# Optimization experiments

Hardware: AMD Instinct MI355X
Metric: run time of the kernel (lower is better)

Reference implementation:

```python
import jax, jax.numpy as jnp
import numpy as np

N = 100000
E = 1600000
G = 64  # number of graphs
EPS = 1e-5
NEG_SLOPE = 0.2


def _gat_conv(x, W, a_src, a_dst, b, src, dst, n, H, C):
    # x: [n, in]; W: [in, H*C]; a_src/a_dst: [H, C]; b: [H*C]
    h = (x @ W).reshape(n, H, C)                      # [n,H,C]
    al_s = jnp.sum(h * a_src, axis=-1)                # [n,H]
    al_d = jnp.sum(h * a_dst, axis=-1)                # [n,H]
    score = jax.nn.leaky_relu(al_s[src] + al_d[dst], NEG_SLOPE)  # [E,H]
    # segment softmax over incoming edges of each dst node
    m = jax.ops.segment_max(score, dst, num_segments=n)
    ex = jnp.exp(score - jax.lax.stop_gradient(m)[dst])
    den = jax.ops.segment_sum(ex, dst, num_segments=n)
    alpha = ex / den[dst]                             # [E,H]
    out = jax.ops.segment_sum(alpha[:, :, None] * h[src], dst, num_segments=n)
    return out.reshape(n, H * C) + b


def _bn_relu(x, gamma, beta):
    mu = jnp.mean(x, axis=0)
    var = jnp.var(x, axis=0)  # biased, matches torch BN normalization
    return jax.nn.relu((x - mu) * jax.lax.rsqrt(var + EPS) * gamma + beta)


def setup_inputs() -> dict:
    key = jax.random.key(0)
    ks = jax.random.split(key, 32)
    d = {}
    d['x'] = jax.random.normal(ks[0], (N, 3), dtype=jnp.float32)
    d['edge_index'] = jax.random.randint(ks[1], (2, E), 0, N, dtype=jnp.int64)
    d['batch'] = jnp.sort(jax.random.randint(ks[2], (N,), 0, G, dtype=jnp.int64))
    def p(k, shape):
        return jax.random.normal(k, shape, dtype=jnp.float32) * 0.1
    # conv1: 3 -> 16, heads=2
    d['W1'] = p(ks[3], (3, 32)); d['as1'] = p(ks[4], (2, 16)); d['ad1'] = p(ks[5], (2, 16)); d['b1'] = p(ks[6], (32,))
    d['g1'] = jnp.ones((32,), jnp.float32); d['be1'] = jnp.zeros((32,), jnp.float32)
    # conv2: 32 -> 32, heads=2
    d['W2'] = p(ks[7], (32, 64)); d['as2'] = p(ks[8], (2, 32)); d['ad2'] = p(ks[9], (2, 32)); d['b2'] = p(ks[10], (64,))
    d['g2'] = jnp.ones((64,), jnp.float32); d['be2'] = jnp.zeros((64,), jnp.float32)
    # conv3: 64 -> 64, heads=2
    d['W3'] = p(ks[11], (64, 128)); d['as3'] = p(ks[12], (2, 64)); d['ad3'] = p(ks[13], (2, 64)); d['b3'] = p(ks[14], (128,))
    d['g3'] = jnp.ones((128,), jnp.float32); d['be3'] = jnp.zeros((128,), jnp.float32)
    d['fcw'] = p(ks[15], (128, 10)); d['fcb'] = p(ks[16], (10,))
    return d


def reference(x, edge_index, batch, W1, as1, ad1, b1, g1, be1, W2, as2, ad2, b2, g2, be2, W3, as3, ad3, b3, g3, be3, fcw, fcb):
    n = x.shape[0]
    loops = jnp.arange(n, dtype=edge_index.dtype)  # PyG GATConv add_self_loops=True
    src = jnp.concatenate([edge_index[0], loops])
    dst = jnp.concatenate([edge_index[1], loops])
    h = _bn_relu(_gat_conv(x, W1, as1, ad1, b1, src, dst, n, 2, 16), g1, be1)
    h = _bn_relu(_gat_conv(h, W2, as2, ad2, b2, src, dst, n, 2, 32), g2, be2)
    h = _bn_relu(_gat_conv(h, W3, as3, ad3, b3, src, dst, n, 2, 64), g3, be3)
    pooled = jax.ops.segment_max(h, batch, num_segments=G)  # [G,128]
    return pooled @ fcw + fcb
```

## Files before the change

### kernel.cpp

```cpp
#include <hip/hip_runtime.h>
#include <cstddef>

constexpr int NN = 100000;
constexpr int NE = 1600000;
constexpr int TE = NE + NN;
constexpr int NG = 64;
constexpr float EPS = 1e-5f;
constexpr float NEG_SLOPE = 0.2f;
constexpr int NREP = 16;

constexpr int NBUCK = 256;
constexpr int DPB = 391;
constexpr int PHB = 256;
constexpr int CH = (TE + PHB - 1) / PHB;

typedef __attribute__((ext_vector_type(8))) short bf16x8;
typedef __attribute__((ext_vector_type(4))) float f32x4;

__device__ __forceinline__ unsigned short f2bf(float f) {
    unsigned u = __float_as_uint(f);
    u += 0x7fffu + ((u >> 16) & 1u);
    return (unsigned short)(u >> 16);
}
__device__ __forceinline__ float bf2f(unsigned short s) {
    return __uint_as_float((unsigned)s << 16);
}
__device__ __forceinline__ float bflo(unsigned u) { return __uint_as_float(u << 16); }
__device__ __forceinline__ float bfhi(unsigned u) { return __uint_as_float(u & 0xffff0000u); }
__device__ __forceinline__ void unpack8(uint4 v, float* f) {
    f[0] = bflo(v.x); f[1] = bfhi(v.x); f[2] = bflo(v.y); f[3] = bfhi(v.y);
    f[4] = bflo(v.z); f[5] = bfhi(v.z); f[6] = bflo(v.w); f[7] = bfhi(v.w);
}
__device__ __forceinline__ uint4 pack8(const float* o) {
    uint4 pk;
    pk.x = (unsigned)f2bf(o[0]) | ((unsigned)f2bf(o[1]) << 16);
    pk.y = (unsigned)f2bf(o[2]) | ((unsigned)f2bf(o[3]) << 16);
    pk.z = (unsigned)f2bf(o[4]) | ((unsigned)f2bf(o[5]) << 16);
    pk.w = (unsigned)f2bf(o[6]) | ((unsigned)f2bf(o[7]) << 16);
    return pk;
}
__device__ __forceinline__ bf16x8 ld_bf8(const unsigned short* p) {
    union { uint4 u; bf16x8 b; } cv;
    cv.u = *(const uint4*)p;
    return cv.b;
}
__device__ __forceinline__ float lrelu(float v) { return v > 0.f ? v : NEG_SLOPE * v; }


__global__ void k_hist(const int* __restrict__ ei, int* __restrict__ hist) {
    __shared__ int hcnt[NBUCK];
    for (int i = threadIdx.x; i < NBUCK; i += 256) hcnt[i] = 0;
    __syncthreads();
    int k = blockIdx.x;
    int e0 = k * CH, e1 = min(e0 + CH, TE);
    for (int e = e0 + threadIdx.x; e < e1; e += 256) {
        int d = (e < NE) ? ei[NE + e] : (e - NE);
        atomicAdd(&hcnt[d / DPB], 1);
    }
    __syncthreads();
    for (int b = threadIdx.x; b < NBUCK; b += 256) hist[b * PHB + k] = hcnt[b];
}

__global__ void k_scanA(int* __restrict__ hist, int* __restrict__ bsum) {
    __shared__ int ls[PHB];
    int b = blockIdx.x, t = threadIdx.x;
    int v = hist[b * PHB + t];
    ls[t] = v;
    __syncthreads();
    for (int off = 1; off < PHB; off <<= 1) {
        int add = (t >= off) ? ls[t - off] : 0;
        __syncthreads();
        ls[t] += add;
        __syncthreads();
    }
    hist[b * PHB + t] = ls[t] - v;
    if (t == PHB - 1) bsum[b] = ls[t];
}

__global__ void k_scanB(const int* __restrict__ bsum, int* __restrict__ bbase,
                        int* __restrict__ rowptr) {
    __shared__ int ls[NBUCK];
    int t = threadIdx.x;
    int v = bsum[t];
    ls[t] = v;
    __syncthreads();
    for (int off = 1; off < NBUCK; off <<= 1) {
        int add = (t >= off) ? ls[t - off] : 0;
        __syncthreads();
        ls[t] += add;
        __syncthreads();
    }
    bbase[t] = ls[t] - v;
    if (t == NBUCK - 1) { bbase[NBUCK] = ls[t]; rowptr[NN] = ls[t]; }
}

__global__ void k_scatter(const int* __restrict__ ei, const int* __restrict__ hist,
                          const int* __restrict__ bbase, int* __restrict__ pairs) {
    __shared__ int cur[NBUCK];
    int k = blockIdx.x;
    for (int b = threadIdx.x; b < NBUCK; b += 256) cur[b] = bbase[b] + hist[b * PHB + k];
    __syncthreads();
    int e0 = k * CH, e1 = min(e0 + CH, TE);
    for (int e = e0 + threadIdx.x; e < e1; e += 256) {
        int s, d;
        if (e < NE) { s = ei[e]; d = ei[NE + e]; } else { s = e - NE; d = s; }
        int b = d / DPB, ld = d - b * DPB;
        int pos = atomicAdd(&cur[b], 1);
        pairs[pos] = (s << 9) | ld;
    }
}

__global__ void k_csr(const int* __restrict__ pairs, const int* __restrict__ bbase,
                      int* __restrict__ rowptr, int* __restrict__ colsrc) {
    __shared__ int deg[DPB];
    __shared__ int exc[DPB];
    __shared__ int sc[512];
    int b = blockIdx.x, t = threadIdx.x;
    int base = bbase[b], cnt = bbase[b + 1] - base;
    int d0 = b * DPB;
    int ndst = min(DPB, NN - d0);
    for (int i = t; i < DPB; i += 256) deg[i] = 0;
    __syncthreads();
    for (int i = t; i < cnt; i += 256) atomicAdd(&deg[pairs[base + i] & 511], 1);
    __syncthreads();
    sc[t] = (t < DPB) ? deg[t] : 0;
    sc[t + 256] = (t + 256 < DPB) ? deg[t + 256] : 0;
    __syncthreads();
    for (int off = 1; off < 512; off <<= 1) {
        int a0 = (t >= off) ? sc[t - off] : 0;
        int a1 = (t + 256 >= off) ? sc[t + 256 - off] : 0;
        __syncthreads();
        sc[t] += a0; sc[t + 256] += a1;
        __syncthreads();
    }
    if (t < DPB) exc[t] = sc[t] - deg[t];
    if (t + 256 < DPB) exc[t + 256] = sc[t + 256] - deg[t + 256];
    __syncthreads();
    for (int i = t; i < ndst; i += 256) rowptr[d0 + i] = base + exc[i];
    for (int i = t; i < DPB; i += 256) deg[i] = 0;
    __syncthreads();
    for (int i = t; i < cnt; i += 256) {
        int p = pairs[base + i];
        int ld = p & 511;
        int s = (unsigned)p >> 9;
        int pos = base + exc[ld] + atomicAdd(&deg[ld], 1);
        colsrc[pos] = s;
    }
}


__global__ void k_wa(const float* __restrict__ W1, const float* __restrict__ as1,
                     const float* __restrict__ ad1,
                     const float* __restrict__ W2, const float* __restrict__ as2,
                     const float* __restrict__ ad2,
                     const float* __restrict__ W3, const float* __restrict__ as3,
                     const float* __restrict__ ad3,
                     float* __restrict__ was1, float* __restrict__ wad1,
                     float* __restrict__ was2, float* __restrict__ wad2,
                     float* __restrict__ was3, float* __restrict__ wad3) {
    int t = threadIdx.x;
    if (t < 6) {
        int h = t / 3, i = t % 3;
        float s = 0.f, d = 0.f;
        for (int c = 0; c < 16; ++c) {
            float w = W1[i * 32 + h * 16 + c];
            s += w * as1[h * 16 + c];
            d += w * ad1[h * 16 + c];
        }
        was1[t] = s; wad1[t] = d;
    }
    if (t < 64) {
        int h = t / 32, i = t % 32;
        float s = 0.f, d = 0.f;
        for (int c = 0; c < 32; ++c) {
            float w = W2[i * 64 + h * 32 + c];
            s += w * as2[h * 32 + c];
            d += w * ad2[h * 32 + c];
        }
        was2[t] = s; wad2[t] = d;
    }
    if (t < 128) {
        int h = t / 64, i = t % 64;
        float s = 0.f, d = 0.f;
        for (int c = 0; c < 64; ++c) {
            float w = W3[i * 128 + h * 64 + c];
            s += w * as3[h * 64 + c];
            d += w * ad3[h * 64 + c];
        }
        was3[t] = s; wad3[t] = d;
    }
}


__global__ void k_wsplit(const float* __restrict__ W2, const float* __restrict__ W3,
                         unsigned short* __restrict__ w2hi, unsigned short* __restrict__ w2lo,
                         unsigned short* __restrict__ w3hi, unsigned short* __restrict__ w3lo) {
    int t = blockIdx.x * 256 + threadIdx.x;
    if (t < 2048) {
        int c = t / 32, i = t % 32;
        float w = W2[i * 64 + c];
        unsigned short hi = f2bf(w);
        float lo = w - bf2f(hi);
        w2hi[c * 32 + i] = hi;
        w2lo[c * 32 + i] = f2bf(lo);
    }
    if (t < 8192) {
        int c = t / 64, i = t % 64;
        float w = W3[i * 128 + c];
        unsigned short hi = f2bf(w);
        float lo = w - bf2f(hi);
        w3hi[c * 64 + i] = hi;
        w3lo[c * 64 + i] = f2bf(lo);
    }
}


__global__ void k_logits1(const float* __restrict__ x, const float* __restrict__ was,
                          const float* __restrict__ wad, float* __restrict__ als,
                          float* __restrict__ ald) {
    int n = blockIdx.x * 256 + threadIdx.x;
    if (n >= NN) return;
    float x0 = x[n * 3], x1 = x[n * 3 + 1], x2 = x[n * 3 + 2];
    als[n * 2 + 0] = x0 * was[0] + x1 * was[1] + x2 * was[2];
    als[n * 2 + 1] = x0 * was[3] + x1 * was[4] + x2 * was[5];
    ald[n * 2 + 0] = x0 * wad[0] + x1 * wad[1] + x2 * wad[2];
    ald[n * 2 + 1] = x0 * wad[3] + x1 * wad[4] + x2 * wad[5];
}


template <int IN>
__global__ void k_prep(const unsigned short* __restrict__ x,
                       const float* __restrict__ bnrep,
                       const float* __restrict__ gamma, const float* __restrict__ beta,
                       const float* __restrict__ was, const float* __restrict__ wad,
                       unsigned short* __restrict__ xbn,
                       float* __restrict__ als, float* __restrict__ ald) {
    constexpr int P = IN / 8;
    __shared__ float sbn[2 * IN];
    __shared__ float swa[4 * IN];
    if (threadIdx.x < IN) {
        int c = threadIdx.x;
        float s = 0.f, ss = 0.f;
#pragma unroll
        for (int r = 0; r < NREP; ++r) {
            s  += bnrep[r * 2 * IN + c];
            ss += bnrep[r * 2 * IN + IN + c];
        }
        float mu = s / NN;
        float var = ss / NN - mu * mu;
        float sca = gamma[c] * rsqrtf(var + EPS);
        sbn[c] = sca;
        sbn[IN + c] = beta[c] - mu * sca;
    }
    for (int i = threadIdx.x; i < 2 * IN; i += 256) {
        swa[i] = was[i];
        swa[2 * IN + i] = wad[i];
    }
    __syncthreads();
    int idx = blockIdx.x * 256 + threadIdx.x;
    int node = idx / P, pl = idx % P;
    if (node >= NN) return;
    uint4 v = *(const uint4*)&x[(size_t)node * IN + pl * 8];
    float f[8];
    unpack8(v, f);
    float s0 = 0.f, s1 = 0.f, d0 = 0.f, d1 = 0.f;
#pragma unroll
    for (int k = 0; k < 8; ++k) {
        int c = pl * 8 + k;
        float t = f[k] * sbn[c] + sbn[IN + c];
        t = t > 0.f ? t : 0.f;
        f[k] = t;
        s0 += t * swa[c];           s1 += t * swa[IN + c];
        d0 += t * swa[2 * IN + c];  d1 += t * swa[3 * IN + c];
    }
    *(uint4*)&xbn[(size_t)node * IN + pl * 8] = pack8(f);
#pragma unroll
    for (int m = 1; m < P; m <<= 1) {
        s0 += __shfl_xor(s0, m, 64); s1 += __shfl_xor(s1, m, 64);
        d0 += __shfl_xor(d0, m, 64); d1 += __shfl_xor(d1, m, 64);
    }
    if (pl == 0) {
        als[node * 2 + 0] = s0; als[node * 2 + 1] = s1;
        ald[node * 2 + 0] = d0; ald[node * 2 + 1] = d1;
    }
}


template <int IN>
__global__ void k_agg(const int* __restrict__ rowptr, const int* __restrict__ colsrc,
                      const unsigned short* __restrict__ x,
                      const float* __restrict__ als, const float* __restrict__ ald,
                      unsigned short* __restrict__ agg) {
    constexpr int LPE = IN / 8;
    constexpr int EPI2 = 32 / LPE;
    constexpr int UNR = 2;
    __shared__ float4 etab[4][64];
    int wv = threadIdx.x >> 6, lane = threadIdx.x & 63;
    int hw = lane >> 5, hl = lane & 31;
    int base = ((int)blockIdx.x * 4 + wv) * 2;
    int wid = base + hw;
    bool valid = wid < NN;
    int start = 0, cnt = 0;
    float2 dv = make_float2(0.f, 0.f);
    if (valid) {
        start = rowptr[wid];
        cnt = rowptr[wid + 1] - start;
        dv = ((const float2*)ald)[wid];
    }
    int mc = max(cnt, __shfl_xor(cnt, 32, 64));

    if (mc <= 32) {
        int e = start + hl;
        bool act = valid && (hl < cnt);
        int s = act ? colsrc[e] : 0;
        float2 av = act ? ((const float2*)als)[s] : make_float2(0.f, 0.f);
        float t0 = act ? lrelu(av.x + dv.x) : -1e30f;
        float t1 = act ? lrelu(av.y + dv.y) : -1e30f;
        float m0 = t0, m1 = t1;
#pragma unroll
        for (int off = 16; off; off >>= 1) {
            m0 = fmaxf(m0, __shfl_xor(m0, off, 32));
            m1 = fmaxf(m1, __shfl_xor(m1, off, 32));
        }
        float w0 = act ? __expf(t0 - m0) : 0.f;
        float w1 = act ? __expf(t1 - m1) : 0.f;
        float den0 = w0, den1 = w1;
#pragma unroll
        for (int off = 16; off; off >>= 1) {
            den0 += __shfl_xor(den0, off, 32);
            den1 += __shfl_xor(den1, off, 32);
        }
        float i0 = valid ? 1.f / den0 : 0.f;
        float i1 = valid ? 1.f / den1 : 0.f;
        etab[wv][lane] = make_float4(__int_as_float(s), w0 * i0, w1 * i1, 0.f);
        int sub = hl / LPE, cl = hl % LPE;
        float a0[8], a1[8];
#pragma unroll
        for (int k = 0; k < 8; ++k) { a0[k] = 0.f; a1[k] = 0.f; }
        if (valid) {
            int cm1 = cnt - 1;
            for (int j0 = 0; j0 < cnt; j0 += EPI2 * UNR) {
                float l0[UNR], l1[UNR];
                uint4 hv[UNR];
#pragma unroll
                for (int u = 0; u < UNR; ++u) {
                    int jj = j0 + u * EPI2 + sub;
                    int jc = min(jj, cm1);
                    float4 ed = etab[wv][hw * 32 + jc];
                    bool on = jj <= cm1;
                    l0[u] = on ? ed.y : 0.f;
                    l1[u] = on ? ed.z : 0.f;
                    hv[u] = *(const uint4*)&x[(size_t)__float_as_int(ed.x) * IN + cl * 8];
                }
#pragma unroll
                for (int u = 0; u < UNR; ++u) {
                    float f[8];
                    unpack8(hv[u], f);
#pragma unroll
                    for (int k = 0; k < 8; ++k) {
                        a0[k] += l0[u] * f[k];
                        a1[k] += l1[u] * f[k];
                    }
                }
            }
        }
#pragma unroll
        for (int m = LPE; m < 32; m <<= 1) {
#pragma unroll
            for (int k = 0; k < 8; ++k) {
                a0[k] += __shfl_xor(a0[k], m, 64);
                a1[k] += __shfl_xor(a1[k], m, 64);
            }
        }
        if (valid && sub == 0) {
            *(uint4*)&agg[(size_t)wid * 2 * IN + cl * 8] = pack8(a0);
            *(uint4*)&agg[(size_t)wid * 2 * IN + IN + cl * 8] = pack8(a1);
        }
    } else {
        for (int i2 = 0; i2 < 2; ++i2) {
            int w2 = base + i2;
            if (w2 >= NN) continue;
            int st = rowptr[w2], en = rowptr[w2 + 1];
            float2 dv2 = ((const float2*)ald)[w2];
            float m0 = -1e30f, m1 = -1e30f;
            for (int e = st + lane; e < en; e += 64) {
                int s = colsrc[e];
                m0 = fmaxf(m0, lrelu(als[s * 2 + 0] + dv2.x));
                m1 = fmaxf(m1, lrelu(als[s * 2 + 1] + dv2.y));
            }
#pragma unroll
            for (int off = 32; off; off >>= 1) {
                m0 = fmaxf(m0, __shfl_xor(m0, off, 64));
                m1 = fmaxf(m1, __shfl_xor(m1, off, 64));
            }
            float den0 = 0.f, den1 = 0.f;
            for (int e = st + lane; e < en; e += 64) {
                int s = colsrc[e];
                den0 += __expf(lrelu(als[s * 2 + 0] + dv2.x) - m0);
                den1 += __expf(lrelu(als[s * 2 + 1] + dv2.y) - m1);
            }
#pragma unroll
            for (int off = 32; off; off >>= 1) {
                den0 += __shfl_xor(den0, off, 64);
                den1 += __shfl_xor(den1, off, 64);
            }
            float inv0 = 1.f / den0, inv1 = 1.f / den1;
            int c = lane;
            float a0 = 0.f, a1 = 0.f;
            for (int e = st; e < en; ++e) {
                int s = colsrc[e];
                float aa0 = __expf(lrelu(als[s * 2 + 0] + dv2.x) - m0) * inv0;
                float aa1 = __expf(lrelu(als[s * 2 + 1] + dv2.y) - m1) * inv1;
                if (c < IN) {
                    float vv = bf2f(x[(size_t)s * IN + c]);
                    a0 += aa0 * vv;
                    a1 += aa1 * vv;
                }
            }
            if (c < IN) {
                agg[(size_t)w2 * 2 * IN + c] = f2bf(a0);
                agg[(size_t)w2 * 2 * IN + IN + c] = f2bf(a1);
            }
        }
    }
}

__global__ void k_agg1(const int* __restrict__ rowptr, const int* __restrict__ colsrc,
                       const float* __restrict__ x, const float* __restrict__ als,
                       const float* __restrict__ ald, float* __restrict__ agg) {
    int wv = threadIdx.x >> 6, lane = threadIdx.x & 63;
    int hw = lane >> 5, hl = lane & 31;
    int base = ((int)blockIdx.x * 4 + wv) * 2;
    int wid = base + hw;
    bool valid = wid < NN;
    int start = 0, cnt = 0;
    float2 dv = make_float2(0.f, 0.f);
    if (valid) {
        start = rowptr[wid];
        cnt = rowptr[wid + 1] - start;
        dv = ((const float2*)ald)[wid];
    }
    int mc = max(cnt, __shfl_xor(cnt, 32, 64));
    if (mc <= 32) {
        int e = start + hl;
        bool act = valid && (hl < cnt);
        int s = act ? colsrc[e] : 0;
        float2 av = act ? ((const float2*)als)[s] : make_float2(0.f, 0.f);
        float t0 = act ? lrelu(av.x + dv.x) : -1e30f;
        float t1 = act ? lrelu(av.y + dv.y) : -1e30f;
        float m0 = t0, m1 = t1;
#pragma unroll
        for (int off = 16; off; off >>= 1) {
            m0 = fmaxf(m0, __shfl_xor(m0, off, 32));
            m1 = fmaxf(m1, __shfl_xor(m1, off, 32));
        }
        float w0 = act ? __expf(t0 - m0) : 0.f;
        float w1 = act ? __expf(t1 - m1) : 0.f;
        float den0 = w0, den1 = w1;
#pragma unroll
        for (int off = 16; off; off >>= 1) {
            den0 += __shfl_xor(den0, off, 32);
            den1 += __shfl_xor(den1, off, 32);
        }
        float a[6];
#pragma unroll
        for (int k = 0; k < 6; ++k) a[k] = 0.f;
        if (act) {
            float al0 = w0 / den0, al1 = w1 / den1;
            float x0 = x[s * 3], x1 = x[s * 3 + 1], x2 = x[s * 3 + 2];
            a[0] = al0 * x0; a[1] = al0 * x1; a[2] = al0 * x2;
            a[3] = al1 * x0; a[4] = al1 * x1; a[5] = al1 * x2;
        }
#pragma unroll
        for (int m = 1; m < 32; m <<= 1) {
#pragma unroll
            for (int k = 0; k < 6; ++k) a[k] += __shfl_xor(a[k], m, 64);
        }
        if (valid && hl == 0) {
#pragma unroll
            for (int k = 0; k < 6; ++k) agg[(size_t)wid * 6 + k] = a[k];
        }
    } else {
        for (int i2 = 0; i2 < 2; ++i2) {
            int w2 = base + i2;
            if (w2 >= NN) continue;
            int st = rowptr[w2], en = rowptr[w2 + 1];
            float2 dv2 = ((const float2*)ald)[w2];
            float m0 = -1e30f, m1 = -1e30f;
            for (int e = st + lane; e < en; e += 64) {
                int s = colsrc[e];
                m0 = fmaxf(m0, lrelu(als[s * 2 + 0] + dv2.x));
                m1 = fmaxf(m1, lrelu(als[s * 2 + 1] + dv2.y));
            }
#pragma unroll
            for (int off = 32; off; off >>= 1) {
                m0 = fmaxf(m0, __shfl_xor(m0, off, 64));
                m1 = fmaxf(m1, __shfl_xor(m1, off, 64));
            }
            float den0 = 0.f, den1 = 0.f;
            for (int e = st + lane; e < en; e += 64) {
                int s = colsrc[e];
                den0 += __expf(lrelu(als[s * 2 + 0] + dv2.x) - m0);
                den1 += __expf(lrelu(als[s * 2 + 1] + dv2.y) - m1);
            }
#pragma unroll
            for (int off = 32; off; off >>= 1) {
                den0 += __shfl_xor(den0, off, 64);
                den1 += __shfl_xor(den1, off, 64);
            }
            float inv0 = 1.f / den0, inv1 = 1.f / den1;
            float a[6];
#pragma unroll
            for (int k = 0; k < 6; ++k) a[k] = 0.f;
            for (int e = st + lane; e < en; e += 64) {
                int s = colsrc[e];
                float aa0 = __expf(lrelu(als[s * 2 + 0] + dv2.x) - m0) * inv0;
                float aa1 = __expf(lrelu(als[s * 2 + 1] + dv2.y) - m1) * inv1;
                float x0 = x[s * 3], x1 = x[s * 3 + 1], x2 = x[s * 3 + 2];
                a[0] += aa0 * x0; a[1] += aa0 * x1; a[2] += aa0 * x2;
                a[3] += aa1 * x0; a[4] += aa1 * x1; a[5] += aa1 * x2;
            }
#pragma unroll
            for (int m = 1; m < 64; m <<= 1) {
#pragma unroll
                for (int k = 0; k < 6; ++k) a[k] += __shfl_xor(a[k], m, 64);
            }
            if (lane == 0) {
#pragma unroll
                for (int k = 0; k < 6; ++k) agg[(size_t)w2 * 6 + k] = a[k];
            }
        }
    }
}


template <int IN, int OUT>
__global__ void k_tmfma(const unsigned short* __restrict__ agg,
                        const unsigned short* __restrict__ whi,
                        const unsigned short* __restrict__ wlo,
                        unsigned short* __restrict__ xout,
                        float* __restrict__ bnrep) {
    constexpr int C = OUT / 2;
    constexpr int NT = C / 16;
    constexpr int KS = IN / 32;
    __shared__ float red[2 * OUT];
    for (int i = threadIdx.x; i < 2 * OUT; i += 256) red[i] = 0.f;
    __syncthreads();
    int wv = threadIdx.x >> 6, l = threadIdx.x & 63;
    int head = wv & 1;
    int node0 = blockIdx.x * 32 + (wv >> 1) * 16;
    int lr = l & 15, kg = l >> 4;
    bf16x8 a[KS];
#pragma unroll
    for (int ks = 0; ks < KS; ++ks)
        a[ks] = ld_bf8(&agg[(size_t)(node0 + lr) * 2 * IN + head * IN + ks * 32 + kg * 8]);
    f32x4 acc[NT];
#pragma unroll
    for (int nt = 0; nt < NT; ++nt) acc[nt] = (f32x4){0.f, 0.f, 0.f, 0.f};
#pragma unroll
    for (int nt = 0; nt < NT; ++nt) {
        int ch = head * C + nt * 16 + lr;
#pragma unroll
        for (int ks = 0; ks < KS; ++ks) {
            bf16x8 bh = ld_bf8(&whi[(size_t)ch * IN + ks * 32 + kg * 8]);
            bf16x8 bl = ld_bf8(&wlo[(size_t)ch * IN + ks * 32 + kg * 8]);
            acc[nt] = __builtin_amdgcn_mfma_f32_16x16x32_bf16(a[ks], bh, acc[nt], 0, 0, 0);
            acc[nt] = __builtin_amdgcn_mfma_f32_16x16x32_bf16(a[ks], bl, acc[nt], 0, 0, 0);
        }
    }
#pragma unroll
    for (int nt = 0; nt < NT; ++nt) {
        int chO = head * C + nt * 16 + lr;
        float s = 0.f, ss = 0.f;
#pragma unroll
        for (int r = 0; r < 4; ++r) {
            float v = acc[nt][r];
            int node = node0 + kg * 4 + r;
            xout[(size_t)node * OUT + chO] = f2bf(v);
            s += v; ss += v * v;
        }
        atomicAdd(&red[chO], s);
        atomicAdd(&red[OUT + chO], ss);
    }
    __syncthreads();
    float* dst = &bnrep[(blockIdx.x & (NREP - 1)) * 2 * OUT];
    for (int i = threadIdx.x; i < 2 * OUT; i += 256) atomicAdd(&dst[i], red[i]);
}

__global__ void k_transform1(const float* __restrict__ agg, const float* __restrict__ W,
                             unsigned short* __restrict__ xout, float* __restrict__ bnrep,
                             int n) {
    __shared__ float xs[32 * 7];
    __shared__ float red[64];
    for (int i = threadIdx.x; i < 64; i += 256) red[i] = 0.f;
    int node0 = blockIdx.x * 32;
    for (int i = threadIdx.x; i < 192; i += 256) {
        int nn = node0 + i / 6;
        float v = (nn < n) ? agg[(size_t)node0 * 6 + i] : 0.f;
        xs[(i / 6) * 7 + (i % 6)] = v;
    }
    __syncthreads();
    int nl = threadIdx.x / 8, q = threadIdx.x % 8;
    int hd = (q >= 4);
    int node = node0 + nl;
    float4 acc = {0.f, 0.f, 0.f, 0.f};
#pragma unroll
    for (int i = 0; i < 3; ++i) {
        float xv = xs[nl * 7 + hd * 3 + i];
        float4 w = *(const float4*)&W[i * 32 + q * 4];
        acc.x += xv * w.x; acc.y += xv * w.y; acc.z += xv * w.z; acc.w += xv * w.w;
    }
    if (node < n) {
        uint2 pk;
        pk.x = (unsigned)f2bf(acc.x) | ((unsigned)f2bf(acc.y) << 16);
        pk.y = (unsigned)f2bf(acc.z) | ((unsigned)f2bf(acc.w) << 16);
        *(uint2*)&xout[(size_t)node * 32 + q * 4] = pk;
        atomicAdd(&red[q * 4 + 0], acc.x); atomicAdd(&red[32 + q * 4 + 0], acc.x * acc.x);
        atomicAdd(&red[q * 4 + 1], acc.y); atomicAdd(&red[32 + q * 4 + 1], acc.y * acc.y);
        atomicAdd(&red[q * 4 + 2], acc.z); atomicAdd(&red[32 + q * 4 + 2], acc.z * acc.z);
        atomicAdd(&red[q * 4 + 3], acc.w); atomicAdd(&red[32 + q * 4 + 3], acc.w * acc.w);
    }
    __syncthreads();
    float* dst = &bnrep[(blockIdx.x & (NREP - 1)) * 64];
    for (int i = threadIdx.x; i < 64; i += 256) atomicAdd(&dst[i], red[i]);
}


__global__ void k_pool(const unsigned short* __restrict__ h, const int* __restrict__ batch,
                       const float* __restrict__ bnrep, const float* __restrict__ gamma,
                       const float* __restrict__ beta, float* __restrict__ pooled, int n) {
    const int K = 32;
    int c = threadIdx.x;
    float s = 0.f, ss = 0.f;
#pragma unroll
    for (int r = 0; r < NREP; ++r) {
        s  += bnrep[r * 256 + c];
        ss += bnrep[r * 256 + 128 + c];
    }
    float mu = s / n;
    float var = ss / n - mu * mu;
    float scale = gamma[c] * rsqrtf(var + EPS);
    float shift = beta[c] - mu * scale;
    int n0 = blockIdx.x * K;
    if (n0 >= n) return;
    int nend = min(n, n0 + K);
    int curg = batch[n0];
    float m = 0.f;
    for (int nn = n0; nn < nend; ++nn) {
        int g = batch[nn];
        if (g != curg) {
            atomicMax((int*)&pooled[curg * 128 + c], __float_as_int(m));
            m = 0.f; curg = g;
        }
        float v = bf2f(h[(size_t)nn * 128 + c]) * scale + shift;
        m = fmaxf(m, v > 0.f ? v : 0.f);
    }
    atomicMax((int*)&pooled[curg * 128 + c], __float_as_int(m));
}

__global__ void k_fc(const float* __restrict__ pooled, const float* __restrict__ fcw,
                     const float* __restrict__ fcb, float* __restrict__ out) {
    int t = threadIdx.x;
    if (t >= NG * 10) return;
    int g = t / 10, j = t % 10;
    float acc = fcb[j];
#pragma unroll
    for (int c = 0; c < 128; ++c) acc += pooled[g * 128 + c] * fcw[c * 10 + j];
    out[g * 10 + j] = acc;
}


extern "C" void kernel_launch(void* const* d_in, const int* in_sizes, int n_in,
                              void* d_out, int out_size, void* d_ws, size_t ws_size,
                              hipStream_t stream) {
    const float* x   = (const float*)d_in[0];
    const int*   ei  = (const int*)d_in[1];
    const int*   bat = (const int*)d_in[2];
    const float* W1  = (const float*)d_in[3];
    const float* as1 = (const float*)d_in[4];
    const float* ad1 = (const float*)d_in[5];
    const float* g1  = (const float*)d_in[7];
    const float* be1 = (const float*)d_in[8];
    const float* W2  = (const float*)d_in[9];
    const float* as2 = (const float*)d_in[10];
    const float* ad2 = (const float*)d_in[11];
    const float* g2  = (const float*)d_in[13];
    const float* be2 = (const float*)d_in[14];
    const float* W3  = (const float*)d_in[15];
    const float* as3 = (const float*)d_in[16];
    const float* ad3 = (const float*)d_in[17];
    const float* g3  = (const float*)d_in[19];
    const float* be3 = (const float*)d_in[20];
    const float* fcw = (const float*)d_in[21];
    const float* fcb = (const float*)d_in[22];
    float* out = (float*)d_out;

    char* w = (char*)d_ws;
    size_t off = 0;
    auto take = [&](size_t bytes) {
        void* p = w + off;
        off += (bytes + 255) & ~(size_t)255;
        return p;
    };
    constexpr size_t ZN = (size_t)NREP * 2 * (32 + 64 + 128) + NG * 128;
    char* zreg = (char*)take(ZN * 4);
    float* bnr1   = (float*)zreg;
    float* bnr2   = bnr1 + NREP * 64;
    float* bnr3   = bnr2 + NREP * 128;
    float* pooled = bnr3 + NREP * 256;

    int*   hist    = (int*)take((size_t)NBUCK * PHB * 4);
    int*   bsum    = (int*)take(NBUCK * 4);
    int*   bbase   = (int*)take((NBUCK + 1) * 4);
    int*   rowptr  = (int*)take((size_t)(NN + 1) * 4);
    int*   pairs   = (int*)take((size_t)TE * 4);
    int*   colsrc  = (int*)take((size_t)TE * 4);
    float* al_s    = (float*)take((size_t)NN * 2 * 4);
    float* al_d    = (float*)take((size_t)NN * 2 * 4);
    float* was1    = (float*)take(64);
    float* wad1    = (float*)take(64);
    float* was2    = (float*)take(64 * 4);
    float* wad2    = (float*)take(64 * 4);
    float* was3    = (float*)take(128 * 4);
    float* wad3    = (float*)take(128 * 4);
    unsigned short* w2hi = (unsigned short*)take(2048 * 2);
    unsigned short* w2lo = (unsigned short*)take(2048 * 2);
    unsigned short* w3hi = (unsigned short*)take(8192 * 2);
    unsigned short* w3lo = (unsigned short*)take(8192 * 2);
    float* agg1f   = (float*)take((size_t)NN * 6 * 4);
    unsigned short* aggb = (unsigned short*)take((size_t)NN * 128 * 2);
    unsigned short* x2   = (unsigned short*)take((size_t)NN * 32 * 2);
    unsigned short* xbn2 = (unsigned short*)take((size_t)NN * 32 * 2);
    unsigned short* x3   = (unsigned short*)take((size_t)NN * 64 * 2);
    unsigned short* xbn3 = (unsigned short*)take((size_t)NN * 64 * 2);
    unsigned short* x4   = (unsigned short*)take((size_t)NN * 128 * 2);

    hipMemsetAsync(zreg, 0, ZN * 4, stream);

    k_hist<<<PHB, 256, 0, stream>>>(ei, hist);
    k_scanA<<<NBUCK, PHB, 0, stream>>>(hist, bsum);
    k_scanB<<<1, NBUCK, 0, stream>>>(bsum, bbase, rowptr);
    k_scatter<<<PHB, 256, 0, stream>>>(ei, hist, bbase, pairs);
    k_csr<<<NBUCK, 256, 0, stream>>>(pairs, bbase, rowptr, colsrc);

    k_wa<<<1, 256, 0, stream>>>(W1, as1, ad1, W2, as2, ad2, W3, as3, ad3,
                                was1, wad1, was2, wad2, was3, wad3);
    k_wsplit<<<32, 256, 0, stream>>>(W2, W3, w2hi, w2lo, w3hi, w3lo);

    const int AGG_BLOCKS = (NN + 7) / 8;

    k_logits1<<<(NN + 255) / 256, 256, 0, stream>>>(x, was1, wad1, al_s, al_d);
    k_agg1<<<AGG_BLOCKS, 256, 0, stream>>>(rowptr, colsrc, x, al_s, al_d, agg1f);
    k_transform1<<<(NN + 31) / 32, 256, 0, stream>>>(agg1f, W1, x2, bnr1, NN);

    k_prep<32><<<(NN * 4 + 255) / 256, 256, 0, stream>>>(x2, bnr1, g1, be1, was2, wad2,
                                                         xbn2, al_s, al_d);
    k_agg<32><<<AGG_BLOCKS, 256, 0, stream>>>(rowptr, colsrc, xbn2, al_s, al_d, aggb);
    k_tmfma<32, 64><<<NN / 32, 256, 0, stream>>>(aggb, w2hi, w2lo, x3, bnr2);

    k_prep<64><<<(NN * 8 + 255) / 256, 256, 0, stream>>>(x3, bnr2, g2, be2, was3, wad3,
                                                         xbn3, al_s, al_d);
    k_agg<64><<<AGG_BLOCKS, 256, 0, stream>>>(rowptr, colsrc, xbn3, al_s, al_d, aggb);
    k_tmfma<64, 128><<<NN / 32, 256, 0, stream>>>(aggb, w3hi, w3lo, x4, bnr3);

    k_pool<<<(NN + 31) / 32, 128, 0, stream>>>(x4, bat, bnr3, g3, be3, pooled, NN);
    k_fc<<<1, 640, 0, stream>>>(pooled, fcw, fcb, out);
}
```

Before: 349.8 us.

## Split fused GAT aggregation into separate alpha and gather kernels

The fused softmax-and-aggregate kernel for layers 2 and 3 is split in two. k_alpha computes per-edge attention weights and writes them to a new TE-sized float2 buffer. k_gather reads colsrc and those weights to do the weighted feature sum. The point is to free the gather kernel from the shared-memory table and the softmax reductions, and to give it a uniform edge loop even for high-degree nodes, which were handled serially before. In exchange it adds an extra launch and a global write and read of about 13.6 MB of edge weights per layer.

Result: faster. 337.9 us (-3.4%).

```diff
diff --git a/kernel.cpp b/kernel.cpp
--- a/kernel.cpp
+++ b/kernel.cpp
@@ -286,15 +286,9 @@
 }
 
 
-template <int IN>
-__global__ void k_agg(const int* __restrict__ rowptr, const int* __restrict__ colsrc,
-                      const unsigned short* __restrict__ x,
-                      const float* __restrict__ als, const float* __restrict__ ald,
-                      unsigned short* __restrict__ agg) {
-    constexpr int LPE = IN / 8;
-    constexpr int EPI2 = 32 / LPE;
-    constexpr int UNR = 2;
-    __shared__ float4 etab[4][64];
+__global__ void k_alpha(const int* __restrict__ rowptr, const int* __restrict__ colsrc,
+                        const float* __restrict__ als, const float* __restrict__ ald,
+                        float2* __restrict__ alf) {
     int wv = threadIdx.x >> 6, lane = threadIdx.x & 63;
     int hw = lane >> 5, hl = lane & 31;
     int base = ((int)blockIdx.x * 4 + wv) * 2;
@@ -330,52 +324,7 @@
             den0 += __shfl_xor(den0, off, 32);
             den1 += __shfl_xor(den1, off, 32);
         }
-        float i0 = valid ? 1.f / den0 : 0.f;
-        float i1 = valid ? 1.f / den1 : 0.f;
-        etab[wv][lane] = make_float4(__int_as_float(s), w0 * i0, w1 * i1, 0.f);
-        int sub = hl / LPE, cl = hl % LPE;
-        float a0[8], a1[8];
-#pragma unroll
-        for (int k = 0; k < 8; ++k) { a0[k] = 0.f; a1[k] = 0.f; }
-        if (valid) {
-            int cm1 = cnt - 1;
-            for (int j0 = 0; j0 < cnt; j0 += EPI2 * UNR) {
-                float l0[UNR], l1[UNR];
-                uint4 hv[UNR];
-#pragma unroll
-                for (int u = 0; u < UNR; ++u) {
-                    int jj = j0 + u * EPI2 + sub;
-                    int jc = min(jj, cm1);
-                    float4 ed = etab[wv][hw * 32 + jc];
-                    bool on = jj <= cm1;
-                    l0[u] = on ? ed.y : 0.f;
-                    l1[u] = on ? ed.z : 0.f;
-                    hv[u] = *(const uint4*)&x[(size_t)__float_as_int(ed.x) * IN + cl * 8];
-                }
-#pragma unroll
-                for (int u = 0; u < UNR; ++u) {
-                    float f[8];
-                    unpack8(hv[u], f);
-#pragma unroll
-                    for (int k = 0; k < 8; ++k) {
-                        a0[k] += l0[u] * f[k];
-                        a1[k] += l1[u] * f[k];
-                    }
-                }
-            }
-        }
-#pragma unroll
-        for (int m = LPE; m < 32; m <<= 1) {
-#pragma unroll
-            for (int k = 0; k < 8; ++k) {
-                a0[k] += __shfl_xor(a0[k], m, 64);
-                a1[k] += __shfl_xor(a1[k], m, 64);
-            }
-        }
-        if (valid && sub == 0) {
-            *(uint4*)&agg[(size_t)wid * 2 * IN + cl * 8] = pack8(a0);
-            *(uint4*)&agg[(size_t)wid * 2 * IN + IN + cl * 8] = pack8(a1);
-        }
+        if (act) alf[e] = make_float2(w0 / den0, w1 / den1);
     } else {
         for (int i2 = 0; i2 < 2; ++i2) {
             int w2 = base + i2;
@@ -405,23 +354,72 @@
                 den1 += __shfl_xor(den1, off, 64);
             }
             float inv0 = 1.f / den0, inv1 = 1.f / den1;
-            int c = lane;
-            float a0 = 0.f, a1 = 0.f;
-            for (int e = st; e < en; ++e) {
+            for (int e = st + lane; e < en; e += 64) {
                 int s = colsrc[e];
-                float aa0 = __expf(lrelu(als[s * 2 + 0] + dv2.x) - m0) * inv0;
-                float aa1 = __expf(lrelu(als[s * 2 + 1] + dv2.y) - m1) * inv1;
-                if (c < IN) {
-                    float vv = bf2f(x[(size_t)s * IN + c]);
-                    a0 += aa0 * vv;
-                    a1 += aa1 * vv;
-                }
-            }
-            if (c < IN) {
-                agg[(size_t)w2 * 2 * IN + c] = f2bf(a0);
-                agg[(size_t)w2 * 2 * IN + IN + c] = f2bf(a1);
-            }
-        }
+                alf[e] = make_float2(__expf(lrelu(als[s * 2 + 0] + dv2.x) - m0) * inv0,
+                                     __expf(lrelu(als[s * 2 + 1] + dv2.y) - m1) * inv1);
+            }
+        }
+    }
+}
+
+
+template <int IN>
+__global__ void k_gather(const int* __restrict__ rowptr, const int* __restrict__ colsrc,
+                         const float2* __restrict__ alf,
+                         const unsigned short* __restrict__ x,
+                         unsigned short* __restrict__ agg) {
+    constexpr int LPE = IN / 8;
+    constexpr int EPI2 = 32 / LPE;
+    constexpr int UNR = 2;
+    int wv = threadIdx.x >> 6, lane = threadIdx.x & 63;
+    int hw = lane >> 5, hl = lane & 31;
+    int wid = ((int)blockIdx.x * 4 + wv) * 2 + hw;
+    if (wid >= NN) return;
+    int start = rowptr[wid];
+    int cnt = rowptr[wid + 1] - start;
+    int sub = hl / LPE, cl = hl % LPE;
+    float a0[8], a1[8];
+#pragma unroll
+    for (int k = 0; k < 8; ++k) { a0[k] = 0.f; a1[k] = 0.f; }
+    int cm1 = cnt - 1;
+    for (int j0 = 0; j0 < cnt; j0 += EPI2 * UNR) {
+        float l0[UNR], l1[UNR];
+        uint4 hv[UNR];
+#pragma unroll
+        for (int u = 0; u < UNR; ++u) {
+            int jj = j0 + u * EPI2 + sub;
+            int jc = min(jj, cm1);
+            int e = start + jc;
+            int s = colsrc[e];
+            float2 al = alf[e];
+            bool on = jj <= cm1;
+            l0[u] = on ? al.x : 0.f;
+            l1[u] = on ? al.y : 0.f;
+            hv[u] = *(const uint4*)&x[(size_t)s * IN + cl * 8];
+        }
+#pragma unroll
+        for (int u = 0; u < UNR; ++u) {
+            float f[8];
+            unpack8(hv[u], f);
+#pragma unroll
+            for (int k = 0; k < 8; ++k) {
+                a0[k] += l0[u] * f[k];
+                a1[k] += l1[u] * f[k];
+            }
+        }
+    }
+#pragma unroll
+    for (int m = LPE; m < 32; m <<= 1) {
+#pragma unroll
+        for (int k = 0; k < 8; ++k) {
+            a0[k] += __shfl_xor(a0[k], m, 64);
+            a1[k] += __shfl_xor(a1[k], m, 64);
+        }
+    }
+    if (sub == 0) {
+        *(uint4*)&agg[(size_t)wid * 2 * IN + cl * 8] = pack8(a0);
+        *(uint4*)&agg[(size_t)wid * 2 * IN + IN + cl * 8] = pack8(a1);
     }
 }
 
@@ -717,6 +715,7 @@
     int*   colsrc  = (int*)take((size_t)TE * 4);
     float* al_s    = (float*)take((size_t)NN * 2 * 4);
     float* al_d    = (float*)take((size_t)NN * 2 * 4);
+    float2* alf    = (float2*)take((size_t)TE * 8);
     float* was1    = (float*)take(64);
     float* wad1    = (float*)take(64);
     float* was2    = (float*)take(64 * 4);
@@ -755,12 +754,14 @@
 
     k_prep<32><<<(NN * 4 + 255) / 256, 256, 0, stream>>>(x2, bnr1, g1, be1, was2, wad2,
                                                          xbn2, al_s, al_d);
-    k_agg<32><<<AGG_BLOCKS, 256, 0, stream>>>(rowptr, colsrc, xbn2, al_s, al_d, aggb);
+    k_alpha<<<AGG_BLOCKS, 256, 0, stream>>>(rowptr, colsrc, al_s, al_d, alf);
+    k_gather<32><<<AGG_BLOCKS, 256, 0, stream>>>(rowptr, colsrc, alf, xbn2, aggb);
     k_tmfma<32, 64><<<NN / 32, 256, 0, stream>>>(aggb, w2hi, w2lo, x3, bnr2);
 
     k_prep<64><<<(NN * 8 + 255) / 256, 256, 0, stream>>>(x3, bnr2, g2, be2, was3, wad3,
                                                          xbn3, al_s, al_d);
-    k_agg<64><<<AGG_BLOCKS, 256, 0, stream>>>(rowptr, colsrc, xbn3, al_s, al_d, aggb);
+    k_alpha<<<AGG_BLOCKS, 256, 0, stream>>>(rowptr, colsrc, al_s, al_d, alf);
+    k_gather<64><<<AGG_BLOCKS, 256, 0, stream>>>(rowptr, colsrc, alf, xbn3, aggb);
     k_tmfma<64, 128><<<NN / 32, 256, 0, stream>>>(aggb, w3hi, w3lo, x4, bnr3);
 
     k_pool<<<(NN + 31) / 32, 128, 0, stream>>>(x4, bat, bnr3, g3, be3, pooled, NN);
```
